# Kernel tuning notes

Hardware: AMD Instinct MI355X
Metric: run time of the kernel (lower is better)

## Reference

```python
import jax, jax.numpy as jnp
import numpy as np

SPATIAL_SHAPES = [(100, 100), (50, 50), (25, 25), (13, 13)]  # (h, w) per level
D_MODEL, N_HEADS, N_LEVELS, N_POINTS = 256, 8, 4, 4
B = 2
S = sum(h * w for h, w in SPATIAL_SHAPES)  # 13294
Q = S  # encoder self-attention: num_queries == sequence_length


def setup_inputs() -> dict:
    key = jax.random.key(0)
    ks = jax.random.split(key, 12)
    d = D_MODEL
    hlp = N_HEADS * N_LEVELS * N_POINTS
    scale = 0.02
    starts = np.cumsum([0] + [h * w for h, w in SPATIAL_SHAPES[:-1]])
    return {
        "hidden_states": jax.random.normal(ks[0], (B, Q, d), jnp.float32),
        "encoder_hidden_states": jax.random.normal(ks[1], (B, S, d), jnp.float32),
        "reference_points": jax.random.uniform(ks[2], (B, Q, N_LEVELS, 2), jnp.float32),
        "W_value": jax.random.normal(ks[3], (d, d), jnp.float32) * scale,
        "b_value": jnp.zeros((d,), jnp.float32),
        "W_off": jax.random.normal(ks[4], (d, hlp * 2), jnp.float32) * scale,
        "b_off": jax.random.normal(ks[5], (hlp * 2,), jnp.float32) * scale,
        "W_attn": jax.random.normal(ks[6], (d, hlp), jnp.float32) * scale,
        "b_attn": jnp.zeros((hlp,), jnp.float32),
        "W_out": jax.random.normal(ks[7], (d, d), jnp.float32) * scale,
        "b_out": jnp.zeros((d,), jnp.float32),
        "spatial_shapes": jnp.asarray(SPATIAL_SHAPES, jnp.int32),
        "level_start_index": jnp.asarray(starts, jnp.int32),
    }


def bilinear_sample(img, grid):
    # img: [N, C, h, w]; grid: [N, Q, P, 2] xy in [-1, 1]
    # F.grid_sample(mode='bilinear', padding_mode='zeros', align_corners=False)
    N, C, h, w = img.shape
    Qg, Pg = grid.shape[1], grid.shape[2]
    x = ((grid[..., 0] + 1.0) * w - 1.0) * 0.5
    y = ((grid[..., 1] + 1.0) * h - 1.0) * 0.5
    x0 = jnp.floor(x)
    y0 = jnp.floor(y)
    x1 = x0 + 1.0
    y1 = y0 + 1.0
    wx1 = x - x0
    wx0 = 1.0 - wx1
    wy1 = y - y0
    wy0 = 1.0 - wy1
    img_flat = img.reshape(N, C, h * w)

    def gather(xi, yi):
        valid = (xi >= 0) & (xi <= w - 1) & (yi >= 0) & (yi <= h - 1)
        xi_c = jnp.clip(xi, 0, w - 1).astype(jnp.int32)
        yi_c = jnp.clip(yi, 0, h - 1).astype(jnp.int32)
        idx = (yi_c * w + xi_c).reshape(N, 1, Qg * Pg)
        vals = jnp.take_along_axis(img_flat, idx, axis=2)  # [N, C, Q*P]
        return vals * valid.reshape(N, 1, Qg * Pg).astype(img.dtype)

    out = (
        gather(x0, y0) * (wx0 * wy0).reshape(N, 1, -1)
        + gather(x1, y0) * (wx1 * wy0).reshape(N, 1, -1)
        + gather(x0, y1) * (wx0 * wy1).reshape(N, 1, -1)
        + gather(x1, y1) * (wx1 * wy1).reshape(N, 1, -1)
    )
    return out.reshape(N, C, Qg, Pg)


def reference(hidden_states, encoder_hidden_states, reference_points,
              W_value, b_value, W_off, b_off, W_attn, b_attn, W_out, b_out,
              spatial_shapes, level_start_index):
    Bq, Qn, d = hidden_states.shape
    H, L, P = N_HEADS, N_LEVELS, N_POINTS
    Dh = d // H
    value = (encoder_hidden_states @ W_value + b_value).reshape(Bq, -1, H, Dh)
    off = (hidden_states @ W_off + b_off).reshape(Bq, Qn, H, L, P, 2)
    aw = (hidden_states @ W_attn + b_attn).reshape(Bq, Qn, H, L * P)
    aw = jax.nn.softmax(aw, axis=-1).reshape(Bq, Qn, H, L, P)
    # offset normalizer is (width, height) per level
    norm = jnp.stack([spatial_shapes[:, 1], spatial_shapes[:, 0]], -1).astype(off.dtype)
    loc = reference_points[:, :, None, :, None, :] + off / norm[None, None, None, :, None, :]
    grids = 2.0 * loc - 1.0  # [B, Q, H, L, P, 2]

    starts = np.cumsum([0] + [h * w for h, w in SPATIAL_SHAPES])
    sampled = []
    for lvl, (h, w) in enumerate(SPATIAL_SHAPES):
        v = value[:, starts[lvl]:starts[lvl + 1]]              # [B, h*w, H, Dh]
        v = v.transpose(0, 2, 3, 1).reshape(Bq * H, Dh, h, w)   # [B*H, Dh, h, w]
        g = grids[:, :, :, lvl].transpose(0, 2, 1, 3, 4).reshape(Bq * H, Qn, P, 2)
        sampled.append(bilinear_sample(v, g))                   # [B*H, Dh, Q, P]
    samp = jnp.stack(sampled, axis=-2).reshape(Bq * H, Dh, Qn, L * P)
    wts = aw.transpose(0, 2, 1, 3, 4).reshape(Bq * H, 1, Qn, L * P)
    out = (samp * wts).sum(-1)                                  # [B*H, Dh, Q]
    out = out.reshape(Bq, H * Dh, Qn).transpose(0, 2, 1)        # [B, Q, d]
    out = out @ W_out + b_out
    return out, aw
```

## Files before the change

kernel.cpp:

```cpp
#include <hip/hip_runtime.h>
#include <math.h>

#define BQn 2
#define QN 13294
#define SN 13294
#define NH 8
#define DH 32
#define DM 256

typedef __attribute__((ext_vector_type(8))) short short8;
typedef __attribute__((ext_vector_type(4))) float f32x4;

__device__ __forceinline__ unsigned short f2bf(float x) {
    union { float f; unsigned int u; } c; c.f = x;
    unsigned int r = c.u + 0x7fff + ((c.u >> 16) & 1);
    return (unsigned short)(r >> 16);
}
__device__ __forceinline__ float bf2f(unsigned short u) {
    union { unsigned int i; float f; } c; c.i = ((unsigned int)u) << 16;
    return c.f;
}

__global__ __launch_bounds__(256) void conv_x(
    const float* __restrict__ in, unsigned short* __restrict__ out, int n)
{
    const int i = (blockIdx.x * 256 + threadIdx.x) * 4;
    if (i >= n) return;
    const float4 v = *(const float4*)(in + i);
    ushort4 o;
    o.x = f2bf(v.x); o.y = f2bf(v.y); o.z = f2bf(v.z); o.w = f2bf(v.w);
    *(ushort4*)(out + i) = o;
}

__global__ __launch_bounds__(256) void conv_weights(
    const float* __restrict__ Wv, const float* __restrict__ Woff,
    const float* __restrict__ Wa, const float* __restrict__ Wout,
    unsigned short* __restrict__ WvT, unsigned short* __restrict__ WoffT,
    unsigned short* __restrict__ WaT, unsigned short* __restrict__ WoutT)
{
    const int t = blockIdx.x * 256 + threadIdx.x;
    if (t < 65536) {
        const int n = t & 255, k = t >> 8;
        WvT[(size_t)n * 256 + k] = f2bf(Wv[(size_t)k * 256 + n]);
    } else if (t < 131072) {
        const int i = t - 65536, n = i & 255, k = i >> 8;
        WoffT[(size_t)n * 256 + k] = f2bf(Woff[(size_t)k * 256 + n]);
    } else if (t < 163840) {
        const int i = t - 131072, n = i & 127, k = i >> 7;
        WaT[(size_t)n * 256 + k] = f2bf(Wa[(size_t)k * 128 + n]);
    } else if (t < 229376) {
        const int i = t - 163840, n = i & 255, k = i >> 8;
        WoutT[(size_t)n * 256 + k] = f2bf(Wout[(size_t)k * 256 + n]);
    }
}

template<int N, int MODE>
__global__ __launch_bounds__(256) void gemm_mfma(
    const unsigned short* __restrict__ A,
    const unsigned short* __restrict__ WT,
    const float* __restrict__ bias,
    void* __restrict__ Cv, int M)
{
    __shared__ unsigned short As[128][72];
    __shared__ unsigned short Bs[64][72];
    const int tid  = threadIdx.x;
    const int lane = tid & 63, wid = tid >> 6;
    const int wr = wid >> 1, wc = wid & 1;
    const int r0 = blockIdx.y * 128, n0 = blockIdx.x * 64;

    f32x4 acc[4][2] = {};

    for (int k0 = 0; k0 < 256; k0 += 64) {
        #pragma unroll
        for (int i = 0; i < 4; ++i) {
            const int idx = i * 256 + tid;
            const int row = idx >> 3, ch = (idx & 7) << 3;
            int grow = r0 + row; if (grow >= M) grow = M - 1;
            *(uint4*)&As[row][ch] =
                *(const uint4*)(A + (size_t)grow * 256 + k0 + ch);
        }
        #pragma unroll
        for (int i = 0; i < 2; ++i) {
            const int idx = i * 256 + tid;
            const int row = idx >> 3, ch = (idx & 7) << 3;
            *(uint4*)&Bs[row][ch] =
                *(const uint4*)(WT + (size_t)(n0 + row) * 256 + k0 + ch);
        }
        __syncthreads();
        #pragma unroll
        for (int kk = 0; kk < 2; ++kk) {
            const int kb = kk * 32 + (lane >> 4) * 8;
            short8 bfr[2];
            #pragma unroll
            for (int n = 0; n < 2; ++n)
                bfr[n] = *(const short8*)&Bs[wc * 32 + n * 16 + (lane & 15)][kb];
            #pragma unroll
            for (int m = 0; m < 4; ++m) {
                const short8 afr =
                    *(const short8*)&As[wr * 64 + m * 16 + (lane & 15)][kb];
                #pragma unroll
                for (int n = 0; n < 2; ++n)
                    acc[m][n] = __builtin_amdgcn_mfma_f32_16x16x32_bf16(
                        afr, bfr[n], acc[m][n], 0, 0, 0);
            }
        }
        __syncthreads();
    }

    #pragma unroll
    for (int m = 0; m < 4; ++m)
        #pragma unroll
        for (int n = 0; n < 2; ++n) {
            const int col = n0 + wc * 32 + n * 16 + (lane & 15);
            #pragma unroll
            for (int j = 0; j < 4; ++j) {
                const int row = r0 + wr * 64 + m * 16 + (lane >> 4) * 4 + j;
                if (row >= M) continue;
                const float v = acc[m][n][j] + bias[col];
                if (MODE == 0) {
                    ((float*)Cv)[(size_t)row * N + col] = v;
                } else {
                    const int b = row / SN, s = row - b * SN;
                    const int h = col >> 5, dh = col & 31;
                    ((unsigned short*)Cv)
                        [(((size_t)b * NH + h) * SN + s) * DH + dh] = f2bf(v);
                }
            }
        }
}

__global__ __launch_bounds__(256) void ms_sample(
    const unsigned short* __restrict__ value,
    const float* __restrict__ off,
    const float* __restrict__ awpre,
    const float* __restrict__ refp,
    unsigned short* __restrict__ outh,
    float* __restrict__ awout)
{
    const int h  = blockIdx.x & 7;
    const int qc = blockIdx.x >> 3;
    const int lc = threadIdx.x & 7;
    const int bq = qc * 32 + (threadIdx.x >> 3);
    if (bq >= BQn * QN) return;
    const int b  = bq / QN;
    const int wl = threadIdx.x & 63;
    const int gbase = wl & 56;

    const float2 lw2 = *(const float2*)(awpre + (size_t)bq * 128 + h * 16 + lc * 2);
    float m = fmaxf(lw2.x, lw2.y);
    #pragma unroll
    for (int d = 1; d < 8; d <<= 1) m = fmaxf(m, __shfl_xor(m, d, 8));
    float e0 = expf(lw2.x - m), e1 = expf(lw2.y - m);
    float s = e0 + e1;
    #pragma unroll
    for (int d = 1; d < 8; d <<= 1) s += __shfl_xor(s, d, 8);
    const float inv = 1.f / s;
    e0 *= inv; e1 *= inv;
    *(float2*)(awout + (size_t)bq * 128 + h * 16 + lc * 2) = make_float2(e0, e1);

    const float4 o4 = *(const float4*)(off + (size_t)bq * 256 + h * 32 + lc * 4);
    const int lvl = lc >> 1;
    const float2 rp = *(const float2*)(refp + (size_t)bq * 8 + lvl * 2);
    const float fw = (lvl == 0) ? 100.f : (lvl == 1) ? 50.f : (lvl == 2) ? 25.f : 13.f;
    const float lx0 = rp.x + o4.x / fw, ly0 = rp.y + o4.y / fw;
    const float lx1 = rp.x + o4.z / fw, ly1 = rp.y + o4.w / fw;

    float ax = 0.f, ay = 0.f, az = 0.f, aw_ = 0.f;
    const unsigned short* vplane = value + (((size_t)b * NH + h) * SN) * DH + lc * 4;

    #pragma unroll
    for (int p = 0; p < 16; ++p) {
        constexpr int LW[4]  = {100, 50, 25, 13};
        constexpr int LST[4] = {0, 10000, 12500, 13125};
        const int l  = p >> 2;
        const int w  = LW[l];
        const int hh = LW[l];
        const int st = LST[l];
        const int src = gbase + (p >> 1);
        const float lx = __shfl((p & 1) ? lx1 : lx0, src, 64);
        const float ly = __shfl((p & 1) ? ly1 : ly0, src, 64);
        const float wt = __shfl((p & 1) ? e1  : e0,  src, 64);

        const float x = lx * (float)w - 0.5f;
        const float y = ly * (float)hh - 0.5f;
        const float x0f = floorf(x), y0f = floorf(y);
        const int x0 = (int)x0f, y0 = (int)y0f;
        const float wx1 = x - x0f, wx0 = 1.f - wx1;
        const float wy1 = y - y0f, wy0 = 1.f - wy1;

        #pragma unroll
        for (int c = 0; c < 4; ++c) {
            const int xi = x0 + (c & 1);
            const int yi = y0 + (c >> 1);
            const float cw = ((c & 1) ? wx1 : wx0) * ((c >> 1) ? wy1 : wy0);
            if (xi >= 0 && xi < w && yi >= 0 && yi < hh) {
                const float wgt = cw * wt;
                const ushort4 v =
                    *(const ushort4*)(vplane + (size_t)(st + yi * w + xi) * DH);
                ax  = fmaf(wgt, bf2f(v.x), ax);
                ay  = fmaf(wgt, bf2f(v.y), ay);
                az  = fmaf(wgt, bf2f(v.z), az);
                aw_ = fmaf(wgt, bf2f(v.w), aw_);
            }
        }
    }

    ushort4 o;
    o.x = f2bf(ax); o.y = f2bf(ay); o.z = f2bf(az); o.w = f2bf(aw_);
    *(ushort4*)(outh + (size_t)bq * 256 + h * 32 + lc * 4) = o;
}

extern "C" void kernel_launch(void* const* d_in, const int* in_sizes, int n_in,
                              void* d_out, int out_size, void* d_ws, size_t ws_size,
                              hipStream_t stream) {
    const float* hs   = (const float*)d_in[0];
    const float* enc  = (const float*)d_in[1];
    const float* refp = (const float*)d_in[2];
    const float* Wv   = (const float*)d_in[3];
    const float* bv   = (const float*)d_in[4];
    const float* Woff = (const float*)d_in[5];
    const float* boff = (const float*)d_in[6];
    const float* Wa   = (const float*)d_in[7];
    const float* ba   = (const float*)d_in[8];
    const float* Wout = (const float*)d_in[9];
    const float* bout = (const float*)d_in[10];

    float* out    = (float*)d_out;
    float* aw_out = out + (size_t)BQn * QN * 256;

    const size_t MQ = (size_t)BQn * QN;
    unsigned short* valueb = (unsigned short*)d_ws;
    float* offb  = (float*)(valueb + MQ * 256);
    float* awpre = offb + MQ * 256;
    unsigned short* xb    = (unsigned short*)(awpre + MQ * 128);
    unsigned short* outh  = xb + MQ * 256;
    unsigned short* WvT   = outh + MQ * 256;
    unsigned short* WoffT = WvT  + 256 * 256;
    unsigned short* WaT   = WoffT + 256 * 256;
    unsigned short* WoutT = WaT  + 128 * 256;

    const int M = (int)MQ;
    const dim3 blk(256);
    const int nA = M * 256;
    const int cgrid = (nA / 4 + 255) / 256;

    conv_weights<<<896, blk, 0, stream>>>(Wv, Woff, Wa, Wout,
                                          WvT, WoffT, WaT, WoutT);

    const int my = (M + 127) / 128;
    conv_x<<<cgrid, blk, 0, stream>>>(enc, xb, nA);
    gemm_mfma<256, 1><<<dim3(4, my), blk, 0, stream>>>(xb, WvT,   bv,   valueb, M);
    conv_x<<<cgrid, blk, 0, stream>>>(hs, xb, nA);
    gemm_mfma<256, 0><<<dim3(4, my), blk, 0, stream>>>(xb, WoffT, boff, offb,  M);
    gemm_mfma<128, 0><<<dim3(2, my), blk, 0, stream>>>(xb, WaT,   ba,   awpre, M);

    const int qchunks = (M + 31) / 32;
    ms_sample<<<8 * qchunks, blk, 0, stream>>>(valueb, offb, awpre, refp,
                                               outh, aw_out);

    gemm_mfma<256, 0><<<dim3(4, my), blk, 0, stream>>>(outh, WoutT, bout, out, M);
}
```

Measured before the change: 159.9 us.

## Fuse bf16 input conversion into GEMMs and merge offset/attention projections

Removes the two separate fp32-to-bf16 conversion kernels by converting A tiles on the fly while loading them into shared memory. Concatenates the offset and attention-weight weight matrices so a single 384-wide GEMM writes an interleaved offaw buffer, which the sampler then reads. The sampler also becomes branchless: it clamps coordinates and zeroes invalid corner weights, and it uses multiply-by-reciprocal and fast exp. Trade-offs are redundant fp32 reads of A across the N-tile blocks and extra loads for the out-of-bounds corners that were previously skipped.

After: 142.8 us. -10.7%, faster.

```diff
diff --git a/kernel.cpp b/kernel.cpp
--- a/kernel.cpp
+++ b/kernel.cpp
@@ -1,4 +1,5 @@
 #include <hip/hip_runtime.h>
+#include <hip/hip_bf16.h>
 #include <math.h>
 
 #define BQn 2
@@ -16,20 +17,8 @@
     unsigned int r = c.u + 0x7fff + ((c.u >> 16) & 1);
     return (unsigned short)(r >> 16);
 }
-__device__ __forceinline__ float bf2f(unsigned short u) {
-    union { unsigned int i; float f; } c; c.i = ((unsigned int)u) << 16;
-    return c.f;
-}
-
-__global__ __launch_bounds__(256) void conv_x(
-    const float* __restrict__ in, unsigned short* __restrict__ out, int n)
-{
-    const int i = (blockIdx.x * 256 + threadIdx.x) * 4;
-    if (i >= n) return;
-    const float4 v = *(const float4*)(in + i);
-    ushort4 o;
-    o.x = f2bf(v.x); o.y = f2bf(v.y); o.z = f2bf(v.z); o.w = f2bf(v.w);
-    *(ushort4*)(out + i) = o;
+__device__ __forceinline__ float asf(unsigned int u) {
+    union { unsigned int i; float f; } c; c.i = u; return c.f;
 }
 
 __global__ __launch_bounds__(256) void conv_weights(
@@ -54,11 +43,12 @@
     }
 }
 
-template<int N, int MODE>
+template<int N, int MODE, bool AF32>
 __global__ __launch_bounds__(256) void gemm_mfma(
-    const unsigned short* __restrict__ A,
+    const void* __restrict__ Av,
     const unsigned short* __restrict__ WT,
-    const float* __restrict__ bias,
+    const float* __restrict__ bias0,
+    const float* __restrict__ bias1,
     void* __restrict__ Cv, int M)
 {
     __shared__ unsigned short As[128][72];
@@ -76,8 +66,21 @@
             const int idx = i * 256 + tid;
             const int row = idx >> 3, ch = (idx & 7) << 3;
             int grow = r0 + row; if (grow >= M) grow = M - 1;
-            *(uint4*)&As[row][ch] =
-                *(const uint4*)(A + (size_t)grow * 256 + k0 + ch);
+            if (AF32) {
+                const float* Af = (const float*)Av;
+                const float4 v0 = *(const float4*)(Af + (size_t)grow * 256 + k0 + ch);
+                const float4 v1 = *(const float4*)(Af + (size_t)grow * 256 + k0 + ch + 4);
+                union { __hip_bfloat162 b[4]; uint4 u; } pk;
+                pk.b[0] = __float22bfloat162_rn(make_float2(v0.x, v0.y));
+                pk.b[1] = __float22bfloat162_rn(make_float2(v0.z, v0.w));
+                pk.b[2] = __float22bfloat162_rn(make_float2(v1.x, v1.y));
+                pk.b[3] = __float22bfloat162_rn(make_float2(v1.z, v1.w));
+                *(uint4*)&As[row][ch] = pk.u;
+            } else {
+                const unsigned short* Ab = (const unsigned short*)Av;
+                *(uint4*)&As[row][ch] =
+                    *(const uint4*)(Ab + (size_t)grow * 256 + k0 + ch);
+            }
         }
         #pragma unroll
         for (int i = 0; i < 2; ++i) {
@@ -112,15 +115,16 @@
         #pragma unroll
         for (int n = 0; n < 2; ++n) {
             const int col = n0 + wc * 32 + n * 16 + (lane & 15);
+            const float bsv = (col < 256) ? bias0[col] : bias1[col - 256];
             #pragma unroll
             for (int j = 0; j < 4; ++j) {
                 const int row = r0 + wr * 64 + m * 16 + (lane >> 4) * 4 + j;
                 if (row >= M) continue;
-                const float v = acc[m][n][j] + bias[col];
+                const float v = acc[m][n][j] + bsv;
                 if (MODE == 0) {
                     ((float*)Cv)[(size_t)row * N + col] = v;
                 } else {
-                    const int b = row / SN, s = row - b * SN;
+                    const int b = (row >= SN), s = row - b * SN;
                     const int h = col >> 5, dh = col & 31;
                     ((unsigned short*)Cv)
                         [(((size_t)b * NH + h) * SN + s) * DH + dh] = f2bf(v);
@@ -131,8 +135,7 @@
 
 __global__ __launch_bounds__(256) void ms_sample(
     const unsigned short* __restrict__ value,
-    const float* __restrict__ off,
-    const float* __restrict__ awpre,
+    const float* __restrict__ offaw,
     const float* __restrict__ refp,
     unsigned short* __restrict__ outh,
     float* __restrict__ awout)
@@ -142,15 +145,16 @@
     const int lc = threadIdx.x & 7;
     const int bq = qc * 32 + (threadIdx.x >> 3);
     if (bq >= BQn * QN) return;
-    const int b  = bq / QN;
-    const int wl = threadIdx.x & 63;
-    const int gbase = wl & 56;
-
-    const float2 lw2 = *(const float2*)(awpre + (size_t)bq * 128 + h * 16 + lc * 2);
+    const int b  = (bq >= QN);
+    const int gbase = threadIdx.x & 56;
+
+    const float* rowp = offaw + (size_t)bq * 384;
+
+    const float2 lw2 = *(const float2*)(rowp + 256 + h * 16 + lc * 2);
     float m = fmaxf(lw2.x, lw2.y);
     #pragma unroll
     for (int d = 1; d < 8; d <<= 1) m = fmaxf(m, __shfl_xor(m, d, 8));
-    float e0 = expf(lw2.x - m), e1 = expf(lw2.y - m);
+    float e0 = __expf(lw2.x - m), e1 = __expf(lw2.y - m);
     float s = e0 + e1;
     #pragma unroll
     for (int d = 1; d < 8; d <<= 1) s += __shfl_xor(s, d, 8);
@@ -158,15 +162,17 @@
     e0 *= inv; e1 *= inv;
     *(float2*)(awout + (size_t)bq * 128 + h * 16 + lc * 2) = make_float2(e0, e1);
 
-    const float4 o4 = *(const float4*)(off + (size_t)bq * 256 + h * 32 + lc * 4);
+    const float4 o4 = *(const float4*)(rowp + h * 32 + lc * 4);
     const int lvl = lc >> 1;
     const float2 rp = *(const float2*)(refp + (size_t)bq * 8 + lvl * 2);
-    const float fw = (lvl == 0) ? 100.f : (lvl == 1) ? 50.f : (lvl == 2) ? 25.f : 13.f;
-    const float lx0 = rp.x + o4.x / fw, ly0 = rp.y + o4.y / fw;
-    const float lx1 = rp.x + o4.z / fw, ly1 = rp.y + o4.w / fw;
+    const float rw = (lvl == 0) ? 0.01f : (lvl == 1) ? 0.02f
+                   : (lvl == 2) ? 0.04f : (1.0f / 13.0f);
+    const float lx0 = fmaf(o4.x, rw, rp.x), ly0 = fmaf(o4.y, rw, rp.y);
+    const float lx1 = fmaf(o4.z, rw, rp.x), ly1 = fmaf(o4.w, rw, rp.y);
 
     float ax = 0.f, ay = 0.f, az = 0.f, aw_ = 0.f;
-    const unsigned short* vplane = value + (((size_t)b * NH + h) * SN) * DH + lc * 4;
+    const unsigned short* vplane =
+        value + (((size_t)b * NH + h) * SN) * DH + lc * 4;
 
     #pragma unroll
     for (int p = 0; p < 16; ++p) {
@@ -174,15 +180,14 @@
         constexpr int LST[4] = {0, 10000, 12500, 13125};
         const int l  = p >> 2;
         const int w  = LW[l];
-        const int hh = LW[l];
         const int st = LST[l];
         const int src = gbase + (p >> 1);
         const float lx = __shfl((p & 1) ? lx1 : lx0, src, 64);
         const float ly = __shfl((p & 1) ? ly1 : ly0, src, 64);
         const float wt = __shfl((p & 1) ? e1  : e0,  src, 64);
 
-        const float x = lx * (float)w - 0.5f;
-        const float y = ly * (float)hh - 0.5f;
+        const float x = fmaf(lx, (float)w, -0.5f);
+        const float y = fmaf(ly, (float)w, -0.5f);
         const float x0f = floorf(x), y0f = floorf(y);
         const int x0 = (int)x0f, y0 = (int)y0f;
         const float wx1 = x - x0f, wx0 = 1.f - wx1;
@@ -193,15 +198,17 @@
             const int xi = x0 + (c & 1);
             const int yi = y0 + (c >> 1);
             const float cw = ((c & 1) ? wx1 : wx0) * ((c >> 1) ? wy1 : wy0);
-            if (xi >= 0 && xi < w && yi >= 0 && yi < hh) {
-                const float wgt = cw * wt;
-                const ushort4 v =
-                    *(const ushort4*)(vplane + (size_t)(st + yi * w + xi) * DH);
-                ax  = fmaf(wgt, bf2f(v.x), ax);
-                ay  = fmaf(wgt, bf2f(v.y), ay);
-                az  = fmaf(wgt, bf2f(v.z), az);
-                aw_ = fmaf(wgt, bf2f(v.w), aw_);
-            }
+            const bool valid = ((unsigned)xi < (unsigned)w) &
+                               ((unsigned)yi < (unsigned)w);
+            const float wgt = valid ? cw * wt : 0.f;
+            const int xc = min(max(xi, 0), w - 1);
+            const int yc = min(max(yi, 0), w - 1);
+            const uint2 v =
+                *(const uint2*)(vplane + (size_t)(st + yc * w + xc) * DH);
+            ax  = fmaf(wgt, asf(v.x << 16),          ax);
+            ay  = fmaf(wgt, asf(v.x & 0xffff0000u),  ay);
+            az  = fmaf(wgt, asf(v.y << 16),          az);
+            aw_ = fmaf(wgt, asf(v.y & 0xffff0000u),  aw_);
         }
     }
 
@@ -230,33 +237,28 @@
 
     const size_t MQ = (size_t)BQn * QN;
     unsigned short* valueb = (unsigned short*)d_ws;
-    float* offb  = (float*)(valueb + MQ * 256);
-    float* awpre = offb + MQ * 256;
-    unsigned short* xb    = (unsigned short*)(awpre + MQ * 128);
-    unsigned short* outh  = xb + MQ * 256;
+    float* offaw = (float*)(valueb + MQ * 256);
+    unsigned short* outh  = (unsigned short*)(offaw + MQ * 384);
     unsigned short* WvT   = outh + MQ * 256;
-    unsigned short* WoffT = WvT  + 256 * 256;
-    unsigned short* WaT   = WoffT + 256 * 256;
-    unsigned short* WoutT = WaT  + 128 * 256;
+    unsigned short* WcatT = WvT + 256 * 256;
+    unsigned short* WoutT = WcatT + 384 * 256;
 
     const int M = (int)MQ;
     const dim3 blk(256);
-    const int nA = M * 256;
-    const int cgrid = (nA / 4 + 255) / 256;
 
     conv_weights<<<896, blk, 0, stream>>>(Wv, Woff, Wa, Wout,
-                                          WvT, WoffT, WaT, WoutT);
+                                          WvT, WcatT, WcatT + 65536, WoutT);
 
     const int my = (M + 127) / 128;
-    conv_x<<<cgrid, blk, 0, stream>>>(enc, xb, nA);
-    gemm_mfma<256, 1><<<dim3(4, my), blk, 0, stream>>>(xb, WvT,   bv,   valueb, M);
-    conv_x<<<cgrid, blk, 0, stream>>>(hs, xb, nA);
-    gemm_mfma<256, 0><<<dim3(4, my), blk, 0, stream>>>(xb, WoffT, boff, offb,  M);
-    gemm_mfma<128, 0><<<dim3(2, my), blk, 0, stream>>>(xb, WaT,   ba,   awpre, M);
+    gemm_mfma<256, 1, true ><<<dim3(4, my), blk, 0, stream>>>(
+        enc, WvT, bv, bv, valueb, M);
+    gemm_mfma<384, 0, true ><<<dim3(6, my), blk, 0, stream>>>(
+        hs, WcatT, boff, ba, offaw, M);
 
     const int qchunks = (M + 31) / 32;
-    ms_sample<<<8 * qchunks, blk, 0, stream>>>(valueb, offb, awpre, refp,
+    ms_sample<<<8 * qchunks, blk, 0, stream>>>(valueb, offaw, refp,
                                                outh, aw_out);
 
-    gemm_mfma<256, 0><<<dim3(4, my), blk, 0, stream>>>(outh, WoutT, bout, out, M);
-}
+    gemm_mfma<256, 0, false><<<dim3(4, my), blk, 0, stream>>>(
+        outh, WoutT, bout, bout, out, M);
+}
```
